# Kernel tuning notes

Hardware: AMD Instinct MI355X
Metric: run time of the kernel (lower is better)

## Reference

```python
import jax, jax.numpy as jnp
import numpy as np

T, B = 64, 2048
LATENT, OBS, CTRL, NMAT, H = 128, 128, 16, 16, 128


def setup_inputs() -> dict:
    key = jax.random.key(0)
    ks = iter(jax.random.split(key, 32))

    def dense(shape, fan_in):
        return jax.random.normal(next(ks), shape, jnp.float32) / np.sqrt(fan_in)

    inp = {
        "xs": jax.random.normal(next(ks), (T, B, OBS), jnp.float32),
        "us": jax.random.normal(next(ks), (T, B, CTRL), jnp.float32),
        "eps1": jax.random.normal(next(ks), (B, LATENT), jnp.float32),
        "eps": jax.random.normal(next(ks), (T - 1, B, LATENT), jnp.float32),
        # InitialNetwork: LSTM(128) + Dense(128) + Dense(2*latent)
        "lstm_Wx": dense((OBS, 4 * H), OBS),
        "lstm_Wh": dense((H, 4 * H), H),
        "lstm_b": jnp.zeros((4 * H,), jnp.float32),
        "init_W1": dense((H, H), H),
        "init_b1": jnp.zeros((H,), jnp.float32),
        "init_W2": dense((H, 2 * LATENT), H),
        "init_b2": jnp.zeros((2 * LATENT,), jnp.float32),
        # InitialTransition
        "trans_W1": dense((LATENT, H), LATENT),
        "trans_b1": jnp.zeros((H,), jnp.float32),
        "trans_W2": dense((H, LATENT), H),
        "trans_b2": jnp.zeros((LATENT,), jnp.float32),
        # Observation
        "obs_W1": dense((LATENT, H), LATENT),
        "obs_b1": jnp.zeros((H,), jnp.float32),
        "obs_W2": dense((H, OBS), H),
        "obs_b2": jnp.zeros((OBS,), jnp.float32),
        # Recognition (input: z ++ x ++ u)
        "rec_W1": dense((LATENT + OBS + CTRL, H), LATENT + OBS + CTRL),
        "rec_b1": jnp.zeros((H,), jnp.float32),
        "rec_W2": dense((H, 2 * LATENT), H),
        "rec_b2": jnp.zeros((2 * LATENT,), jnp.float32),
        # TransitionWeights (no bias, normal(0.01) init)
        "alpha_W": 0.01 * jax.random.normal(next(ks), (LATENT + CTRL, NMAT), jnp.float32),
        # mixture banks
        "A": 0.01 * jax.random.normal(next(ks), (NMAT, LATENT, LATENT), jnp.float32),
        "Bm": 0.01 * jax.random.normal(next(ks), (NMAT, LATENT, CTRL), jnp.float32),
        "C": 0.01 * jax.random.normal(next(ks), (NMAT, OBS, LATENT), jnp.float32),
    }
    return inp


def reference(xs, us, eps1, eps, lstm_Wx, lstm_Wh, lstm_b,
              init_W1, init_b1, init_W2, init_b2,
              trans_W1, trans_b1, trans_W2, trans_b2,
              obs_W1, obs_b1, obs_W2, obs_b2,
              rec_W1, rec_b1, rec_W2, rec_b2,
              alpha_W, A, Bm, C):
    Bsz = xs.shape[1]
    Hd = lstm_Wh.shape[0]

    # --- InitialNetwork: LSTM over time (xs is (T,B,obs); flax transposes to batch-major, net effect is a scan over T) ---
    def lstm_step(carry, x_t):
        c, h = carry
        gates = x_t @ lstm_Wx + h @ lstm_Wh + lstm_b  # (B, 4H)
        i, f, g, o = jnp.split(gates, 4, axis=-1)     # flax gate order i,f,g,o
        c = jax.nn.sigmoid(f) * c + jax.nn.sigmoid(i) * jnp.tanh(g)
        h = jax.nn.sigmoid(o) * jnp.tanh(c)
        return (c, h), None

    zeros = jnp.zeros((Bsz, Hd), xs.dtype)
    (_, h_last), _ = jax.lax.scan(lstm_step, (zeros, zeros), xs)
    hid = jax.nn.relu(h_last @ init_W1 + init_b1)
    w1_mean, w1_logvar = jnp.split(hid @ init_W2 + init_b2, 2, axis=-1)
    w_1 = w1_mean + jnp.exp(w1_logvar / 2) * eps1

    # --- InitialTransition ---
    z_1 = jax.nn.relu(w_1 @ trans_W1 + trans_b1) @ trans_W2 + trans_b2

    def obs_fn(z):
        return jax.nn.relu(z @ obs_W1 + obs_b1) @ obs_W2 + obs_b2

    # --- unrolled DVBF transition as a scan over t = 0..T-2 ---
    def step(z, inp):
        x_next, u_t, eps_t = inp
        x_mean = obs_fn(z)
        r = jax.nn.relu(jnp.concatenate([z, x_next, u_t], axis=-1) @ rec_W1 + rec_b1)
        w_mean, w_logvar = jnp.split(r @ rec_W2 + rec_b2, 2, axis=-1)
        w = w_mean + jnp.exp(w_logvar / 2) * eps_t
        alphas = jax.nn.softmax(jnp.concatenate([z, u_t], axis=-1) @ alpha_W)  # (B, NMAT)
        # fused gating + matrix mixing + matvec (same math as building A_t/B_t/C_t)
        z_next = (jnp.einsum('bi,ijk,bk->bj', alphas, A, z)
                  + jnp.einsum('bi,ijk,bk->bj', alphas, Bm, u_t)
                  + jnp.einsum('bi,ijk,bk->bj', alphas, C, w))
        return z_next, (z_next, x_mean)

    Tn = xs.shape[0]
    _, (zs_rest, x_rec) = jax.lax.scan(step, z_1, (xs[1:], us[:Tn - 1], eps[:Tn - 1]))

    zs = jnp.concatenate([z_1[None], zs_rest], axis=0).reshape(-1, z_1.shape[-1])  # vstack -> (T*B, latent)
    x_rec = x_rec.reshape(-1, x_rec.shape[-1])                                    # ((T-1)*B, obs)
    return zs, x_rec
```

## Files before the change

kernel.cpp:

```cpp
#include <hip/hip_runtime.h>
#include <math.h>

#define TT   64
#define BB   2048
#define OBSN 128
#define CTRLN 16
#define LATN 128
#define NMN  16
#define HDN  128

typedef __attribute__((ext_vector_type(8))) short short8;
typedef __attribute__((ext_vector_type(4))) float f32x4;

__device__ __forceinline__ float sigf(float x) { return 1.0f / (1.0f + expf(-x)); }

__device__ __forceinline__ unsigned short f2bf(float x) {
    unsigned int u = __float_as_uint(x);
    unsigned int r = (u + 0x7fffu + ((u >> 16) & 1u)) >> 16;
    return (unsigned short)r;
}

__device__ __forceinline__ f32x4 mfma16(short8 a, short8 b, f32x4 c) {
    return __builtin_amdgcn_mfma_f32_16x16x32_bf16(a, b, c, 0, 0, 0);
}

__global__ __launch_bounds__(256) void cvt_bf4_k(
    const float* __restrict__ in, unsigned short* __restrict__ out, int n4)
{
    int i = blockIdx.x * 256 + threadIdx.x;
    if (i >= n4) return;
    float4 v = ((const float4*)in)[i];
    ushort4 o;
    o.x = f2bf(v.x); o.y = f2bf(v.y); o.z = f2bf(v.z); o.w = f2bf(v.w);
    ((ushort4*)out)[i] = o;
}

__global__ __launch_bounds__(256) void pack_b_k(
    const float* __restrict__ W, unsigned short* __restrict__ out,
    int K, int N, int KT)
{
    int id = blockIdx.x * 256 + threadIdx.x;
    int total = (N / 16) * KT * 64;
    if (id >= total) return;
    int lane = id & 63;
    int kt = (id >> 6) % KT;
    int nt = id / (64 * KT);
    int n = nt * 16 + (lane & 15);
    int kb = kt * 32 + (lane >> 4) * 8;
#pragma unroll
    for (int j = 0; j < 8; j++) {
        int k = kb + j;
        out[(size_t)id * 8 + j] = (k < K) ? f2bf(W[(size_t)k * N + n]) : (unsigned short)0;
    }
}

__global__ __launch_bounds__(256) void pack_lstm_k(
    const float* __restrict__ Wx, const float* __restrict__ Wh,
    unsigned short* __restrict__ out)
{
    int id = blockIdx.x * 256 + threadIdx.x;
    if (id >= 32 * 8 * 64) return;
    int lane = id & 63;
    int kt = (id >> 6) & 7;
    int nt = id >> 9;
    int n = nt * 16 + (lane & 15);
    int kb = kt * 32 + (lane >> 4) * 8;
#pragma unroll
    for (int j = 0; j < 8; j++) {
        int k = kb + j;
        float v = (k < 128) ? Wx[(size_t)k * 512 + n] : Wh[(size_t)(k - 128) * 512 + n];
        out[(size_t)id * 8 + j] = f2bf(v);
    }
}

__global__ __launch_bounds__(256) void pack_wmix_k(
    const float* __restrict__ A, const float* __restrict__ Bm,
    const float* __restrict__ C, unsigned short* __restrict__ out)
{
    int id = blockIdx.x * 256 + threadIdx.x;
    if (id >= 128 * 9 * 64) return;
    int lane = id & 63;
    int kt = (id >> 6) % 9;
    int nt = id / (64 * 9);
    int c = nt * 16 + (lane & 15);
    int i = c >> 7, jj = c & 127;
    int kb = kt * 32 + (lane >> 4) * 8;
#pragma unroll
    for (int j = 0; j < 8; j++) {
        int k = kb + j;
        float v;
        if (k < 128)      v = A[((size_t)(i * 128 + jj)) * 128 + k];
        else if (k < 144) v = Bm[(size_t)(i * 128 + jj) * 16 + (k - 128)];
        else if (k < 272) v = C[(size_t)(i * 128 + jj) * 128 + (k - 144)];
        else              v = 0.f;
        out[(size_t)id * 8 + j] = f2bf(v);
    }
}

__global__ __launch_bounds__(512, 2) void lstm_k(
    const unsigned short* __restrict__ xs_bf,
    const unsigned short* __restrict__ lstm_pk,
    const float* __restrict__ bias,
    float* __restrict__ hlast)
{
    __shared__ unsigned short wl[13 * 8 * 64 * 8];
    __shared__ unsigned short h_bf[16][136];
    __shared__ float cs[16][128];
    __shared__ float gb[16][516];
    __shared__ float bs[512];

    const int tid = threadIdx.x;
    const int lane = tid & 63;
    const int w = tid >> 6;
    const int quad = lane >> 4;
    const int l15 = lane & 15;
    const int row0 = blockIdx.x * 16;

    short8 bl[19];
#pragma unroll
    for (int f = 0; f < 19; f++) {
        int s = f >> 3, kt = f & 7;
        bl[f] = *(const short8*)&lstm_pk[((((size_t)(w * 4 + s)) * 8 + kt) * 64 + lane) * 8];
    }
#pragma unroll
    for (int f = 19; f < 32; f++) {
        int s = f >> 3, kt = f & 7;
        *(short8*)&wl[(((size_t)w * 13 + (f - 19)) * 64 + lane) * 8] =
            *(const short8*)&lstm_pk[((((size_t)(w * 4 + s)) * 8 + kt) * 64 + lane) * 8];
    }

    bs[tid] = bias[tid];
    for (int idx = tid; idx < 16 * 136; idx += 512) h_bf[idx / 136][idx % 136] = 0;
    for (int idx = tid; idx < 2048; idx += 512) cs[idx >> 7][idx & 127] = 0.f;

    short8 axs[4];
#pragma unroll
    for (int kt = 0; kt < 4; kt++)
        axs[kt] = *(const short8*)&xs_bf[((size_t)(row0 + l15)) * 128 + kt * 32 + quad * 8];
    __syncthreads();

    for (int t = 0; t < TT; t++) {
        short8 a[8];
#pragma unroll
        for (int kt = 0; kt < 4; kt++) a[kt] = axs[kt];
#pragma unroll
        for (int kt = 4; kt < 8; kt++)
            a[kt] = *(const short8*)&h_bf[l15][(kt - 4) * 32 + quad * 8];

        f32x4 D[4];
#pragma unroll
        for (int s = 0; s < 4; s++) D[s] = (f32x4){0.f, 0.f, 0.f, 0.f};
#pragma unroll
        for (int s = 0; s < 4; s++) {
#pragma unroll
            for (int kt = 0; kt < 8; kt++) {
                int f = s * 8 + kt;
                short8 b;
                if (f < 19) b = bl[f];
                else        b = *(const short8*)&wl[(((size_t)w * 13 + (f - 19)) * 64 + lane) * 8];
                D[s] = mfma16(a[kt], b, D[s]);
            }
        }
#pragma unroll
        for (int s = 0; s < 4; s++)
#pragma unroll
            for (int rg = 0; rg < 4; rg++)
                gb[quad * 4 + rg][(w * 4 + s) * 16 + l15] = D[s][rg];
        __syncthreads();

        if (t + 1 < TT) {
#pragma unroll
            for (int kt = 0; kt < 4; kt++)
                axs[kt] = *(const short8*)&xs_bf[((size_t)(t + 1) * 2048 + row0 + l15) * 128 + kt * 32 + quad * 8];
        }
#pragma unroll
        for (int e = 0; e < 4; e++) {
            int idx = tid + e * 512;
            int r = idx >> 7, j = idx & 127;
            float gi = gb[r][j] + bs[j];
            float gf = gb[r][128 + j] + bs[128 + j];
            float gg = gb[r][256 + j] + bs[256 + j];
            float go = gb[r][384 + j] + bs[384 + j];
            float c = sigf(gf) * cs[r][j] + sigf(gi) * tanhf(gg);
            float h = sigf(go) * tanhf(c);
            cs[r][j] = c;
            h_bf[r][j] = f2bf(h);
            if (t == TT - 1) hlast[(size_t)(row0 + r) * 128 + j] = h;
        }
        __syncthreads();
    }
}

__global__ __launch_bounds__(512, 2) void scan_k(
    const unsigned short* __restrict__ xs_bf,
    const unsigned short* __restrict__ us_bf,
    const float* __restrict__ eps,
    const unsigned short* __restrict__ rec1_pk,
    const float* __restrict__ rec_b1,
    const unsigned short* __restrict__ rec2_pk,
    const float* __restrict__ rec_b2,
    const unsigned short* __restrict__ alpha_pk,
    const unsigned short* __restrict__ wmix_pk,
    float* __restrict__ zs)
{
    __shared__ unsigned short amix[16][296];
    __shared__ unsigned short rb_bf[16][136];
    __shared__ float wv[16][260];
    __shared__ float part[8][16][132];
    __shared__ float logits[16][20];
    __shared__ float alph[16][20];
    __shared__ float b1s[128];
    __shared__ float b2s[256];

    const int tid = threadIdx.x;
    const int lane = tid & 63;
    const int w = tid >> 6;
    const int quad = lane >> 4;
    const int l15 = lane & 15;
    const int row0 = blockIdx.x * 16;

    short8 r1f[9];
#pragma unroll
    for (int kt = 0; kt < 9; kt++)
        r1f[kt] = *(const short8*)&rec1_pk[(((size_t)w * 9 + kt) * 64 + lane) * 8];
    short8 r2f[8];
#pragma unroll
    for (int s = 0; s < 2; s++)
#pragma unroll
        for (int kt = 0; kt < 4; kt++)
            r2f[s * 4 + kt] = *(const short8*)&rec2_pk[((((size_t)(2 * w + s)) * 4 + kt) * 64 + lane) * 8];
    short8 alf[5];
#pragma unroll
    for (int kt = 0; kt < 5; kt++)
        alf[kt] = *(const short8*)&alpha_pk[((size_t)kt * 64 + lane) * 8];

    if (tid < 128) b1s[tid] = rec_b1[tid];
    if (tid < 256) b2s[tid] = rec_b2[tid];
    for (int idx = tid; idx < 256; idx += 512)
        amix[idx >> 4][272 + (idx & 15)] = 0;
    for (int idx = tid; idx < 2048; idx += 512) {
        int r = idx >> 7, j = idx & 127;
        amix[r][j] = f2bf(zs[(size_t)(row0 + r) * 128 + j]);
    }
    __syncthreads();

    float ge[4];
    short8 axs[4];

    for (int t = 0; t < TT - 1; t++) {
        if (tid < 256) {
            int r = tid >> 4, c = tid & 15;
            amix[r][128 + c] = us_bf[((size_t)t * 2048 + row0 + r) * 16 + c];
        }
#pragma unroll
        for (int e = 0; e < 4; e++) {
            int idx = tid + e * 512;
            int r = idx >> 7, j = idx & 127;
            ge[e] = eps[((size_t)t * 2048 + row0 + r) * 128 + j];
        }
#pragma unroll
        for (int kt = 0; kt < 4; kt++)
            axs[kt] = *(const short8*)&xs_bf[((size_t)(t + 1) * 2048 + row0 + l15) * 128 + kt * 32 + quad * 8];
        __syncthreads();

        {
            short8 a[9];
#pragma unroll
            for (int kt = 0; kt < 4; kt++)
                a[kt] = *(const short8*)&amix[l15][kt * 32 + quad * 8];
#pragma unroll
            for (int kt = 4; kt < 8; kt++) a[kt] = axs[kt - 4];
            {
                short8 zz = {0, 0, 0, 0, 0, 0, 0, 0};
                a[8] = (quad < 2) ? *(const short8*)&amix[l15][128 + quad * 8] : zz;
            }
            f32x4 D = {0.f, 0.f, 0.f, 0.f};
#pragma unroll
            for (int kt = 0; kt < 9; kt++)
                D = mfma16(a[kt], r1f[kt], D);
            int col = w * 16 + l15;
#pragma unroll
            for (int rg = 0; rg < 4; rg++) {
                float v = fmaxf(D[rg] + b1s[col], 0.f);
                rb_bf[quad * 4 + rg][col] = f2bf(v);
            }
        }
        __syncthreads();

        {
            short8 a[4];
#pragma unroll
            for (int kt = 0; kt < 4; kt++)
                a[kt] = *(const short8*)&rb_bf[l15][kt * 32 + quad * 8];
            f32x4 D0 = {0.f, 0.f, 0.f, 0.f}, D1 = {0.f, 0.f, 0.f, 0.f};
#pragma unroll
            for (int kt = 0; kt < 4; kt++) {
                D0 = mfma16(a[kt], r2f[kt], D0);
                D1 = mfma16(a[kt], r2f[4 + kt], D1);
            }
#pragma unroll
            for (int rg = 0; rg < 4; rg++) {
                wv[quad * 4 + rg][(2 * w) * 16 + l15] = D0[rg];
                wv[quad * 4 + rg][(2 * w + 1) * 16 + l15] = D1[rg];
            }
            if (w == 7) {
                short8 az[5];
#pragma unroll
                for (int kt = 0; kt < 4; kt++)
                    az[kt] = *(const short8*)&amix[l15][kt * 32 + quad * 8];
                short8 zz = {0, 0, 0, 0, 0, 0, 0, 0};
                az[4] = (quad < 2) ? *(const short8*)&amix[l15][128 + quad * 8] : zz;
                f32x4 DL = {0.f, 0.f, 0.f, 0.f};
#pragma unroll
                for (int kt = 0; kt < 5; kt++)
                    DL = mfma16(az[kt], alf[kt], DL);
#pragma unroll
                for (int rg = 0; rg < 4; rg++)
                    logits[quad * 4 + rg][l15] = DL[rg];
            }
        }
        __syncthreads();

        if (tid < 256) {
            int r = tid >> 4, i = tid & 15;
            float x = logits[r][i];
            float m = x;
#pragma unroll
            for (int off = 8; off > 0; off >>= 1)
                m = fmaxf(m, __shfl_xor(m, off, 16));
            float e = expf(x - m);
            float s = e;
#pragma unroll
            for (int off = 8; off > 0; off >>= 1)
                s += __shfl_xor(s, off, 16);
            alph[r][i] = e / s;
        }
#pragma unroll
        for (int e = 0; e < 4; e++) {
            int idx = tid + e * 512;
            int r = idx >> 7, j = idx & 127;
            float mv = wv[r][j] + b2s[j];
            float lv = wv[r][128 + j] + b2s[128 + j];
            float wval = mv + expf(0.5f * lv) * ge[e];
            amix[r][144 + j] = f2bf(wval);
        }
        __syncthreads();

        {
            short8 a[9];
#pragma unroll
            for (int kt = 0; kt < 9; kt++)
                a[kt] = *(const short8*)&amix[l15][kt * 32 + quad * 8];
            const int i0 = 2 * w, i1 = 2 * w + 1;
            float a0[4], a1[4];
#pragma unroll
            for (int rg = 0; rg < 4; rg++) {
                a0[rg] = alph[quad * 4 + rg][i0];
                a1[rg] = alph[quad * 4 + rg][i1];
            }
#pragma unroll 1
            for (int jt = 0; jt < 8; jt++) {
                f32x4 D0 = {0.f, 0.f, 0.f, 0.f}, D1 = {0.f, 0.f, 0.f, 0.f};
#pragma unroll
                for (int kt = 0; kt < 9; kt++) {
                    short8 b0 = *(const short8*)&wmix_pk[((((size_t)i0 * 8 + jt) * 9 + kt) * 64 + lane) * 8];
                    short8 b1 = *(const short8*)&wmix_pk[((((size_t)i1 * 8 + jt) * 9 + kt) * 64 + lane) * 8];
                    D0 = mfma16(a[kt], b0, D0);
                    D1 = mfma16(a[kt], b1, D1);
                }
#pragma unroll
                for (int rg = 0; rg < 4; rg++)
                    part[w][quad * 4 + rg][jt * 16 + l15] = a0[rg] * D0[rg] + a1[rg] * D1[rg];
            }
        }
        __syncthreads();

#pragma unroll
        for (int e = 0; e < 4; e++) {
            int idx = tid + e * 512;
            int r = idx >> 7, j = idx & 127;
            float s = 0.f;
#pragma unroll
            for (int ww = 0; ww < 8; ww++) s += part[ww][r][j];
            zs[((size_t)(t + 1) * 2048 + row0 + r) * 128 + j] = s;
            amix[r][j] = f2bf(s);
        }
        __syncthreads();
    }
}

template <int RELU>
__global__ __launch_bounds__(256) void gemm_bias_k(
    const float* __restrict__ A, const float* __restrict__ W,
    const float* __restrict__ bias, float* __restrict__ Cout,
    int M, int K, int N)
{
    __shared__ float As[16][68];
    __shared__ float Ws[16][64];
    const int tid = threadIdx.x;
    const int row0 = blockIdx.x * 64;
    const int col0 = blockIdx.y * 64;
    const int tx = tid & 15, ty = tid >> 4;
    float acc[4][4];
#pragma unroll
    for (int a = 0; a < 4; a++)
#pragma unroll
        for (int b = 0; b < 4; b++) acc[a][b] = 0.f;

    for (int kc = 0; kc < K; kc += 16) {
        __syncthreads();
#pragma unroll
        for (int e = 0; e < 4; e++) {
            int idx = tid + e * 256;
            int r = idx >> 4, kk = idx & 15;
            As[kk][r] = A[(size_t)(row0 + r) * K + kc + kk];
        }
#pragma unroll
        for (int e = 0; e < 4; e++) {
            int idx = tid + e * 256;
            int kk = idx >> 6, jj = idx & 63;
            Ws[kk][jj] = W[(kc + kk) * N + col0 + jj];
        }
        __syncthreads();
#pragma unroll
        for (int kk = 0; kk < 16; kk++) {
            const float4 a4 = *(const float4*)&As[kk][ty * 4];
            const float4 w4 = *(const float4*)&Ws[kk][tx * 4];
            const float av[4] = {a4.x, a4.y, a4.z, a4.w};
            const float wv2[4] = {w4.x, w4.y, w4.z, w4.w};
#pragma unroll
            for (int r = 0; r < 4; r++)
#pragma unroll
                for (int j = 0; j < 4; j++) acc[r][j] += av[r] * wv2[j];
        }
    }
#pragma unroll
    for (int r = 0; r < 4; r++)
#pragma unroll
        for (int j = 0; j < 4; j++) {
            int gr = row0 + ty * 4 + r, gc = col0 + tx * 4 + j;
            float v = acc[r][j] + bias[gc];
            if (RELU) v = fmaxf(v, 0.f);
            Cout[(size_t)gr * N + gc] = v;
        }
}

__global__ __launch_bounds__(256) void gemm_meanvar_k(
    const float* __restrict__ A, const float* __restrict__ W,
    const float* __restrict__ bias, const float* __restrict__ eps,
    float* __restrict__ out)
{
    __shared__ float As[16][36];
    __shared__ float Ws[16][128];
    const int tid = threadIdx.x;
    const int row0 = blockIdx.x * 32;
    const int j0 = blockIdx.y * 64;
    const int tjx = tid & 31;
    const int trg = tid >> 5;
    float am[4][2], al[4][2];
#pragma unroll
    for (int a = 0; a < 4; a++) { am[a][0] = am[a][1] = 0.f; al[a][0] = al[a][1] = 0.f; }

    for (int kc = 0; kc < 128; kc += 16) {
        __syncthreads();
#pragma unroll
        for (int e = 0; e < 2; e++) {
            int idx = tid + e * 256;
            int r = idx >> 4, kk = idx & 15;
            As[kk][r] = A[(row0 + r) * 128 + kc + kk];
        }
#pragma unroll
        for (int e = 0; e < 2; e++) {
            int idx = tid + e * 256;
            int lin = idx * 4;
            int kk = lin >> 7, cc = lin & 127;
            int half = cc >> 6, jj = cc & 63;
            *(float4*)&Ws[kk][half * 64 + jj] =
                *(const float4*)(W + (kc + kk) * 256 + half * 128 + j0 + jj);
        }
        __syncthreads();
#pragma unroll
        for (int kk = 0; kk < 16; kk++) {
            const float4 a4 = *(const float4*)&As[kk][trg * 4];
            const float2 wm = *(const float2*)&Ws[kk][2 * tjx];
            const float2 wl = *(const float2*)&Ws[kk][64 + 2 * tjx];
            const float av[4] = {a4.x, a4.y, a4.z, a4.w};
#pragma unroll
            for (int rr = 0; rr < 4; rr++) {
                am[rr][0] += av[rr] * wm.x; am[rr][1] += av[rr] * wm.y;
                al[rr][0] += av[rr] * wl.x; al[rr][1] += av[rr] * wl.y;
            }
        }
    }
#pragma unroll
    for (int rr = 0; rr < 4; rr++)
#pragma unroll
        for (int jj = 0; jj < 2; jj++) {
            int r = row0 + trg * 4 + rr;
            int j = j0 + 2 * tjx + jj;
            float m = am[rr][jj] + bias[j];
            float l = al[rr][jj] + bias[128 + j];
            out[r * 128 + j] = m + expf(0.5f * l) * eps[r * 128 + j];
        }
}

__global__ __launch_bounds__(256) void mlp2_k(
    const float* __restrict__ Z, const float* __restrict__ W1,
    const float* __restrict__ b1, const float* __restrict__ W2,
    const float* __restrict__ b2, float* __restrict__ out)
{
    __shared__ float Zs[32][132];
    __shared__ float Hs[32][132];
    __shared__ float Ws[16][128];
    const int tid = threadIdx.x;
    const int row0 = blockIdx.x * 32;
    const int tx = tid & 31;
    const int ty = tid >> 5;

#pragma unroll
    for (int e = 0; e < 4; e++) {
        int idx = tid + e * 256;
        int lin = idx * 4;
        int r = lin >> 7, k = lin & 127;
        *(float4*)&Zs[r][k] = *(const float4*)(Z + (size_t)(row0 + r) * 128 + k);
    }

    float acc[4][4];
#pragma unroll
    for (int a = 0; a < 4; a++)
#pragma unroll
        for (int b = 0; b < 4; b++) acc[a][b] = 0.f;

    for (int kc = 0; kc < 128; kc += 16) {
        __syncthreads();
#pragma unroll
        for (int e = 0; e < 2; e++) {
            int idx = tid + e * 256;
            int lin = idx * 4;
            int kk = lin >> 7, j = lin & 127;
            *(float4*)&Ws[kk][j] = *(const float4*)(W1 + (kc + kk) * 128 + j);
        }
        __syncthreads();
#pragma unroll
        for (int kk = 0; kk < 16; kk++) {
            float av[4];
#pragma unroll
            for (int rr = 0; rr < 4; rr++) av[rr] = Zs[ty * 4 + rr][kc + kk];
            const float4 w4 = *(const float4*)&Ws[kk][tx * 4];
            const float wv2[4] = {w4.x, w4.y, w4.z, w4.w};
#pragma unroll
            for (int r = 0; r < 4; r++)
#pragma unroll
                for (int j = 0; j < 4; j++) acc[r][j] += av[r] * wv2[j];
        }
    }
#pragma unroll
    for (int rr = 0; rr < 4; rr++) {
        float4 hv;
        hv.x = fmaxf(acc[rr][0] + b1[tx * 4 + 0], 0.f);
        hv.y = fmaxf(acc[rr][1] + b1[tx * 4 + 1], 0.f);
        hv.z = fmaxf(acc[rr][2] + b1[tx * 4 + 2], 0.f);
        hv.w = fmaxf(acc[rr][3] + b1[tx * 4 + 3], 0.f);
        *(float4*)&Hs[ty * 4 + rr][tx * 4] = hv;
    }
#pragma unroll
    for (int a = 0; a < 4; a++)
#pragma unroll
        for (int b = 0; b < 4; b++) acc[a][b] = 0.f;

    for (int kc = 0; kc < 128; kc += 16) {
        __syncthreads();
#pragma unroll
        for (int e = 0; e < 2; e++) {
            int idx = tid + e * 256;
            int lin = idx * 4;
            int kk = lin >> 7, j = lin & 127;
            *(float4*)&Ws[kk][j] = *(const float4*)(W2 + (kc + kk) * 128 + j);
        }
        __syncthreads();
#pragma unroll
        for (int kk = 0; kk < 16; kk++) {
            float av[4];
#pragma unroll
            for (int rr = 0; rr < 4; rr++) av[rr] = Hs[ty * 4 + rr][kc + kk];
            const float4 w4 = *(const float4*)&Ws[kk][tx * 4];
            const float wv2[4] = {w4.x, w4.y, w4.z, w4.w};
#pragma unroll
            for (int r = 0; r < 4; r++)
#pragma unroll
                for (int j = 0; j < 4; j++) acc[r][j] += av[r] * wv2[j];
        }
    }
#pragma unroll
    for (int rr = 0; rr < 4; rr++) {
        float4 ov;
        ov.x = acc[rr][0] + b2[tx * 4 + 0];
        ov.y = acc[rr][1] + b2[tx * 4 + 1];
        ov.z = acc[rr][2] + b2[tx * 4 + 2];
        ov.w = acc[rr][3] + b2[tx * 4 + 3];
        *(float4*)(out + (size_t)(row0 + ty * 4 + rr) * 128 + tx * 4) = ov;
    }
}

extern "C" void kernel_launch(void* const* d_in, const int* in_sizes, int n_in,
                              void* d_out, int out_size, void* d_ws, size_t ws_size,
                              hipStream_t stream)
{
    (void)in_sizes; (void)n_in; (void)out_size; (void)ws_size;
    const float* xs       = (const float*)d_in[0];
    const float* us       = (const float*)d_in[1];
    const float* eps1     = (const float*)d_in[2];
    const float* eps      = (const float*)d_in[3];
    const float* lstm_Wx  = (const float*)d_in[4];
    const float* lstm_Wh  = (const float*)d_in[5];
    const float* lstm_b   = (const float*)d_in[6];
    const float* init_W1  = (const float*)d_in[7];
    const float* init_b1  = (const float*)d_in[8];
    const float* init_W2  = (const float*)d_in[9];
    const float* init_b2  = (const float*)d_in[10];
    const float* trans_W1 = (const float*)d_in[11];
    const float* trans_b1 = (const float*)d_in[12];
    const float* trans_W2 = (const float*)d_in[13];
    const float* trans_b2 = (const float*)d_in[14];
    const float* obs_W1   = (const float*)d_in[15];
    const float* obs_b1   = (const float*)d_in[16];
    const float* obs_W2   = (const float*)d_in[17];
    const float* obs_b2   = (const float*)d_in[18];
    const float* rec_W1   = (const float*)d_in[19];
    const float* rec_b1   = (const float*)d_in[20];
    const float* rec_W2   = (const float*)d_in[21];
    const float* rec_b2   = (const float*)d_in[22];
    const float* alpha_W  = (const float*)d_in[23];
    const float* Amat     = (const float*)d_in[24];
    const float* Bmat     = (const float*)d_in[25];
    const float* Cmat     = (const float*)d_in[26];

    float* out  = (float*)d_out;
    float* zs   = out;
    float* xrec = out + (size_t)TT * BB * LATN;

    char* ws = (char*)d_ws;
    unsigned short* xs_bf   = (unsigned short*)(ws);
    unsigned short* us_bf   = (unsigned short*)(ws + 33554432);
    unsigned short* lstm_pk = (unsigned short*)(ws + 37748736);
    unsigned short* rec1_pk = (unsigned short*)(ws + 38010880);
    unsigned short* rec2_pk = (unsigned short*)(ws + 38084608);
    unsigned short* alpha_pk= (unsigned short*)(ws + 38150144);
    unsigned short* wmix_pk = (unsigned short*)(ws + 38155264);
    float* hlast            = (float*)(ws + 39334912);
    float* hidb             = (float*)(ws + 40383488);
    float* w1b              = (float*)(ws + 41432064);
    float* rbg              = (float*)(ws + 42480640);

    cvt_bf4_k<<<16384, 256, 0, stream>>>(xs, xs_bf, 4194304);
    cvt_bf4_k<<<2048, 256, 0, stream>>>(us, us_bf, 524288);
    pack_lstm_k<<<64, 256, 0, stream>>>(lstm_Wx, lstm_Wh, lstm_pk);
    pack_b_k<<<18, 256, 0, stream>>>(rec_W1, rec1_pk, 272, 128, 9);
    pack_b_k<<<16, 256, 0, stream>>>(rec_W2, rec2_pk, 128, 256, 4);
    pack_b_k<<<2, 256, 0, stream>>>(alpha_W, alpha_pk, 144, 16, 5);
    pack_wmix_k<<<288, 256, 0, stream>>>(Amat, Bmat, Cmat, wmix_pk);

    lstm_k<<<128, 512, 0, stream>>>(xs_bf, lstm_pk, lstm_b, hlast);

    gemm_bias_k<1><<<dim3(32, 2), 256, 0, stream>>>(hlast, init_W1, init_b1, hidb, BB, 128, 128);
    gemm_meanvar_k<<<dim3(64, 2), 256, 0, stream>>>(hidb, init_W2, init_b2, eps1, w1b);
    gemm_bias_k<1><<<dim3(32, 2), 256, 0, stream>>>(w1b, trans_W1, trans_b1, rbg, BB, 128, 128);
    gemm_bias_k<0><<<dim3(32, 2), 256, 0, stream>>>(rbg, trans_W2, trans_b2, zs, BB, 128, 128);

    scan_k<<<128, 512, 0, stream>>>(xs_bf, us_bf, eps,
                                    rec1_pk, rec_b1, rec2_pk, rec_b2,
                                    alpha_pk, wmix_pk, zs);

    mlp2_k<<<dim3((TT - 1) * BB / 32), 256, 0, stream>>>(
        zs, obs_W1, obs_b1, obs_W2, obs_b2, xrec);
}
```

Measured before the change: 1.329 ms.

## Overlap A/B mixture matmul with recognition net via warp specialization in scan

The scan kernel splits its warps: four warps compute the alpha-weighted A·z + B·u mixture while the other four run the recognition MLP, so the two independent parts of each step overlap. The mixture weights are split into separate A/B and C packs, the C·w term is computed afterwards by all warps, and the softmax for the next step is computed at the end of the current step. rec_W2 fragments now sit in LDS and several barriers and the logits/wv staging are removed. The cost is load imbalance between the warp groups and more LDS per block, which may lower occupancy.

```diff
diff --git a/kernel.cpp b/kernel.cpp
--- a/kernel.cpp
+++ b/kernel.cpp
@@ -73,15 +73,15 @@
     }
 }
 
-__global__ __launch_bounds__(256) void pack_wmix_k(
+__global__ __launch_bounds__(256) void pack_ab_k(
     const float* __restrict__ A, const float* __restrict__ Bm,
-    const float* __restrict__ C, unsigned short* __restrict__ out)
+    unsigned short* __restrict__ out)
 {
     int id = blockIdx.x * 256 + threadIdx.x;
-    if (id >= 128 * 9 * 64) return;
+    if (id >= 128 * 5 * 64) return;
     int lane = id & 63;
-    int kt = (id >> 6) % 9;
-    int nt = id / (64 * 9);
+    int kt = (id >> 6) % 5;
+    int nt = id / (64 * 5);
     int c = nt * 16 + (lane & 15);
     int i = c >> 7, jj = c & 127;
     int kb = kt * 32 + (lane >> 4) * 8;
@@ -91,9 +91,26 @@
         float v;
         if (k < 128)      v = A[((size_t)(i * 128 + jj)) * 128 + k];
         else if (k < 144) v = Bm[(size_t)(i * 128 + jj) * 16 + (k - 128)];
-        else if (k < 272) v = C[(size_t)(i * 128 + jj) * 128 + (k - 144)];
         else              v = 0.f;
         out[(size_t)id * 8 + j] = f2bf(v);
+    }
+}
+
+__global__ __launch_bounds__(256) void pack_c_k(
+    const float* __restrict__ C, unsigned short* __restrict__ out)
+{
+    int id = blockIdx.x * 256 + threadIdx.x;
+    if (id >= 128 * 4 * 64) return;
+    int lane = id & 63;
+    int kt = (id >> 6) & 3;
+    int nt = id >> 8;
+    int c = nt * 16 + (lane & 15);
+    int i = c >> 7, jj = c & 127;
+    int kb = kt * 32 + (lane >> 4) * 8;
+#pragma unroll
+    for (int j = 0; j < 8; j++) {
+        int k = kb + j;
+        out[(size_t)id * 8 + j] = f2bf(C[((size_t)(i * 128 + jj)) * 128 + k]);
     }
 }
 
@@ -200,15 +217,15 @@
     const unsigned short* __restrict__ rec2_pk,
     const float* __restrict__ rec_b2,
     const unsigned short* __restrict__ alpha_pk,
-    const unsigned short* __restrict__ wmix_pk,
+    const unsigned short* __restrict__ ab_pk,
+    const unsigned short* __restrict__ c_pk,
     float* __restrict__ zs)
 {
     __shared__ unsigned short amix[16][296];
     __shared__ unsigned short rb_bf[16][136];
-    __shared__ float wv[16][260];
-    __shared__ float part[8][16][132];
-    __shared__ float logits[16][20];
-    __shared__ float alph[16][20];
+    __shared__ unsigned short r2lds[16 * 4 * 64 * 8];
+    __shared__ float part1[8][16][16];
+    __shared__ float alph[16][17];
     __shared__ float b1s[128];
     __shared__ float b2s[256];
 
@@ -218,172 +235,259 @@
     const int quad = lane >> 4;
     const int l15 = lane & 15;
     const int row0 = blockIdx.x * 16;
-
-    short8 r1f[9];
-#pragma unroll
-    for (int kt = 0; kt < 9; kt++)
-        r1f[kt] = *(const short8*)&rec1_pk[(((size_t)w * 9 + kt) * 64 + lane) * 8];
-    short8 r2f[8];
-#pragma unroll
-    for (int s = 0; s < 2; s++)
-#pragma unroll
-        for (int kt = 0; kt < 4; kt++)
-            r2f[s * 4 + kt] = *(const short8*)&rec2_pk[((((size_t)(2 * w + s)) * 4 + kt) * 64 + lane) * 8];
+    const int s = w - 4;
+
+    short8 r1f[2][9];
     short8 alf[5];
-#pragma unroll
-    for (int kt = 0; kt < 5; kt++)
-        alf[kt] = *(const short8*)&alpha_pk[((size_t)kt * 64 + lane) * 8];
+    float ge[8];
+    short8 axs[4];
+
+    if (w >= 4) {
+#pragma unroll
+        for (int q = 0; q < 2; q++) {
+            int nt = s + 4 * q;
+#pragma unroll
+            for (int kt = 0; kt < 9; kt++)
+                r1f[q][kt] = *(const short8*)&rec1_pk[(((size_t)nt * 9 + kt) * 64 + lane) * 8];
+        }
+        if (w == 4) {
+#pragma unroll
+            for (int kt = 0; kt < 5; kt++)
+                alf[kt] = *(const short8*)&alpha_pk[((size_t)kt * 64 + lane) * 8];
+        }
+    }
+
+    for (int idx = tid; idx < 4096; idx += 512)
+        ((short8*)r2lds)[idx] = ((const short8*)rec2_pk)[idx];
 
     if (tid < 128) b1s[tid] = rec_b1[tid];
     if (tid < 256) b2s[tid] = rec_b2[tid];
-    for (int idx = tid; idx < 256; idx += 512)
-        amix[idx >> 4][272 + (idx & 15)] = 0;
     for (int idx = tid; idx < 2048; idx += 512) {
         int r = idx >> 7, j = idx & 127;
         amix[r][j] = f2bf(zs[(size_t)(row0 + r) * 128 + j]);
     }
+    if (tid < 256) {
+        int r = tid >> 4, c = tid & 15;
+        amix[r][128 + c] = us_bf[((size_t)(row0 + r)) * 16 + c];
+    }
+    for (int idx = tid; idx < 16 * 152; idx += 512) {
+        int r = idx / 152, j = idx % 152;
+        amix[r][144 + j] = 0;
+    }
     __syncthreads();
 
-    float ge[4];
-    short8 axs[4];
+    if (w == 4) {
+        short8 az[5];
+#pragma unroll
+        for (int kt = 0; kt < 4; kt++)
+            az[kt] = *(const short8*)&amix[l15][kt * 32 + quad * 8];
+        short8 zz = {0, 0, 0, 0, 0, 0, 0, 0};
+        az[4] = (quad < 2) ? *(const short8*)&amix[l15][128 + quad * 8] : zz;
+        f32x4 DL = {0.f, 0.f, 0.f, 0.f};
+#pragma unroll
+        for (int kt = 0; kt < 5; kt++) DL = mfma16(az[kt], alf[kt], DL);
+#pragma unroll
+        for (int rg = 0; rg < 4; rg++) {
+            float x = DL[rg];
+            float m = x;
+#pragma unroll
+            for (int off = 8; off > 0; off >>= 1) m = fmaxf(m, __shfl_xor(m, off, 16));
+            float e = expf(x - m);
+            float ssum = e;
+#pragma unroll
+            for (int off = 8; off > 0; off >>= 1) ssum += __shfl_xor(ssum, off, 16);
+            alph[quad * 4 + rg][l15] = e / ssum;
+        }
+    }
+    if (w >= 4) {
+#pragma unroll
+        for (int jj = 0; jj < 2; jj++)
+#pragma unroll
+            for (int rg = 0; rg < 4; rg++)
+                ge[jj * 4 + rg] = eps[((size_t)(row0 + quad * 4 + rg)) * 128 + (2 * s + jj) * 16 + l15];
+#pragma unroll
+        for (int kt = 0; kt < 4; kt++)
+            axs[kt] = *(const short8*)&xs_bf[((size_t)2048 + row0 + l15) * 128 + kt * 32 + quad * 8];
+    }
+    __syncthreads();
+
+    short8 a1[5];
+    f32x4 accj0, accj1;
 
     for (int t = 0; t < TT - 1; t++) {
-        if (tid < 256) {
-            int r = tid >> 4, c = tid & 15;
-            amix[r][128 + c] = us_bf[((size_t)t * 2048 + row0 + r) * 16 + c];
-        }
-#pragma unroll
-        for (int e = 0; e < 4; e++) {
-            int idx = tid + e * 512;
-            int r = idx >> 7, j = idx & 127;
-            ge[e] = eps[((size_t)t * 2048 + row0 + r) * 128 + j];
-        }
-#pragma unroll
-        for (int kt = 0; kt < 4; kt++)
-            axs[kt] = *(const short8*)&xs_bf[((size_t)(t + 1) * 2048 + row0 + l15) * 128 + kt * 32 + quad * 8];
-        __syncthreads();
-
-        {
-            short8 a[9];
+        if (w < 4) {
+#pragma unroll
+            for (int kt = 0; kt < 5; kt++)
+                a1[kt] = *(const short8*)&amix[l15][kt * 32 + quad * 8];
+            accj0 = (f32x4){0.f, 0.f, 0.f, 0.f};
+            accj1 = (f32x4){0.f, 0.f, 0.f, 0.f};
+#pragma unroll 2
+            for (int i = 0; i < 8; i++) {
+                f32x4 D0 = {0.f, 0.f, 0.f, 0.f}, D1 = {0.f, 0.f, 0.f, 0.f};
+#pragma unroll
+                for (int kt = 0; kt < 5; kt++) {
+                    short8 b0 = *(const short8*)&ab_pk[((((size_t)i * 8 + 2 * w) * 5 + kt) * 64 + lane) * 8];
+                    short8 b1 = *(const short8*)&ab_pk[((((size_t)i * 8 + 2 * w + 1) * 5 + kt) * 64 + lane) * 8];
+                    D0 = mfma16(a1[kt], b0, D0);
+                    D1 = mfma16(a1[kt], b1, D1);
+                }
+#pragma unroll
+                for (int rg = 0; rg < 4; rg++) {
+                    float al = alph[quad * 4 + rg][i];
+                    accj0[rg] += al * D0[rg];
+                    accj1[rg] += al * D1[rg];
+                }
+            }
+        } else {
+            short8 ar[9];
 #pragma unroll
             for (int kt = 0; kt < 4; kt++)
-                a[kt] = *(const short8*)&amix[l15][kt * 32 + quad * 8];
-#pragma unroll
-            for (int kt = 4; kt < 8; kt++) a[kt] = axs[kt - 4];
+                ar[kt] = *(const short8*)&amix[l15][kt * 32 + quad * 8];
+#pragma unroll
+            for (int kt = 4; kt < 8; kt++) ar[kt] = axs[kt - 4];
             {
                 short8 zz = {0, 0, 0, 0, 0, 0, 0, 0};
-                a[8] = (quad < 2) ? *(const short8*)&amix[l15][128 + quad * 8] : zz;
-            }
-            f32x4 D = {0.f, 0.f, 0.f, 0.f};
-#pragma unroll
-            for (int kt = 0; kt < 9; kt++)
-                D = mfma16(a[kt], r1f[kt], D);
-            int col = w * 16 + l15;
+                ar[8] = (quad < 2) ? *(const short8*)&amix[l15][128 + quad * 8] : zz;
+            }
+#pragma unroll
+            for (int q = 0; q < 2; q++) {
+                int nt = s + 4 * q;
+                f32x4 D = {0.f, 0.f, 0.f, 0.f};
+#pragma unroll
+                for (int kt = 0; kt < 9; kt++) D = mfma16(ar[kt], r1f[q][kt], D);
+                int col = nt * 16 + l15;
+#pragma unroll
+                for (int rg = 0; rg < 4; rg++)
+                    rb_bf[quad * 4 + rg][col] = f2bf(fmaxf(D[rg] + b1s[col], 0.f));
+            }
+        }
+        __syncthreads();
+
+        if (w < 4) {
+#pragma unroll 2
+            for (int i = 8; i < 16; i++) {
+                f32x4 D0 = {0.f, 0.f, 0.f, 0.f}, D1 = {0.f, 0.f, 0.f, 0.f};
+#pragma unroll
+                for (int kt = 0; kt < 5; kt++) {
+                    short8 b0 = *(const short8*)&ab_pk[((((size_t)i * 8 + 2 * w) * 5 + kt) * 64 + lane) * 8];
+                    short8 b1 = *(const short8*)&ab_pk[((((size_t)i * 8 + 2 * w + 1) * 5 + kt) * 64 + lane) * 8];
+                    D0 = mfma16(a1[kt], b0, D0);
+                    D1 = mfma16(a1[kt], b1, D1);
+                }
+#pragma unroll
+                for (int rg = 0; rg < 4; rg++) {
+                    float al = alph[quad * 4 + rg][i];
+                    accj0[rg] += al * D0[rg];
+                    accj1[rg] += al * D1[rg];
+                }
+            }
 #pragma unroll
             for (int rg = 0; rg < 4; rg++) {
-                float v = fmaxf(D[rg] + b1s[col], 0.f);
-                rb_bf[quad * 4 + rg][col] = f2bf(v);
+                part1[2 * w][quad * 4 + rg][l15] = accj0[rg];
+                part1[2 * w + 1][quad * 4 + rg][l15] = accj1[rg];
+            }
+        } else {
+            short8 a2[4];
+#pragma unroll
+            for (int kt = 0; kt < 4; kt++)
+                a2[kt] = *(const short8*)&rb_bf[l15][kt * 32 + quad * 8];
+            f32x4 Dm[2], Dl[2];
+#pragma unroll
+            for (int jj = 0; jj < 2; jj++) {
+                int ntm = 2 * s + jj;
+                int ntl = 2 * s + 8 + jj;
+                f32x4 D0 = {0.f, 0.f, 0.f, 0.f}, D1 = {0.f, 0.f, 0.f, 0.f};
+#pragma unroll
+                for (int kt = 0; kt < 4; kt++) {
+                    short8 bm = *(const short8*)&r2lds[(((size_t)ntm * 4 + kt) * 64 + lane) * 8];
+                    short8 bv = *(const short8*)&r2lds[(((size_t)ntl * 4 + kt) * 64 + lane) * 8];
+                    D0 = mfma16(a2[kt], bm, D0);
+                    D1 = mfma16(a2[kt], bv, D1);
+                }
+                Dm[jj] = D0; Dl[jj] = D1;
+            }
+#pragma unroll
+            for (int jj = 0; jj < 2; jj++) {
+                int col = (2 * s + jj) * 16 + l15;
+#pragma unroll
+                for (int rg = 0; rg < 4; rg++) {
+                    float mv = Dm[jj][rg] + b2s[col];
+                    float lv = Dl[jj][rg] + b2s[128 + col];
+                    float wval = mv + expf(0.5f * lv) * ge[jj * 4 + rg];
+                    amix[quad * 4 + rg][144 + col] = f2bf(wval);
+                }
             }
         }
         __syncthreads();
 
         {
-            short8 a[4];
+            short8 a2f[4];
 #pragma unroll
             for (int kt = 0; kt < 4; kt++)
-                a[kt] = *(const short8*)&rb_bf[l15][kt * 32 + quad * 8];
-            f32x4 D0 = {0.f, 0.f, 0.f, 0.f}, D1 = {0.f, 0.f, 0.f, 0.f};
-#pragma unroll
-            for (int kt = 0; kt < 4; kt++) {
-                D0 = mfma16(a[kt], r2f[kt], D0);
-                D1 = mfma16(a[kt], r2f[4 + kt], D1);
+                a2f[kt] = *(const short8*)&amix[l15][144 + kt * 32 + quad * 8];
+            f32x4 accC = {0.f, 0.f, 0.f, 0.f};
+#pragma unroll 2
+            for (int i = 0; i < 16; i++) {
+                f32x4 D = {0.f, 0.f, 0.f, 0.f};
+#pragma unroll
+                for (int kt = 0; kt < 4; kt++) {
+                    short8 b = *(const short8*)&c_pk[((((size_t)i * 8 + w) * 4 + kt) * 64 + lane) * 8];
+                    D = mfma16(a2f[kt], b, D);
+                }
+#pragma unroll
+                for (int rg = 0; rg < 4; rg++)
+                    accC[rg] += alph[quad * 4 + rg][i] * D[rg];
             }
 #pragma unroll
             for (int rg = 0; rg < 4; rg++) {
-                wv[quad * 4 + rg][(2 * w) * 16 + l15] = D0[rg];
-                wv[quad * 4 + rg][(2 * w + 1) * 16 + l15] = D1[rg];
-            }
-            if (w == 7) {
+                int r = quad * 4 + rg;
+                float z = part1[w][r][l15] + accC[rg];
+                zs[((size_t)(t + 1) * 2048 + row0 + r) * 128 + w * 16 + l15] = z;
+                amix[r][w * 16 + l15] = f2bf(z);
+            }
+        }
+        __syncthreads();
+
+        if (t < TT - 2) {
+            if (w == 4) {
                 short8 az[5];
 #pragma unroll
                 for (int kt = 0; kt < 4; kt++)
                     az[kt] = *(const short8*)&amix[l15][kt * 32 + quad * 8];
                 short8 zz = {0, 0, 0, 0, 0, 0, 0, 0};
-                az[4] = (quad < 2) ? *(const short8*)&amix[l15][128 + quad * 8] : zz;
+                az[4] = (quad < 2)
+                    ? *(const short8*)&us_bf[((size_t)(t + 1) * 2048 + row0 + l15) * 16 + quad * 8]
+                    : zz;
                 f32x4 DL = {0.f, 0.f, 0.f, 0.f};
 #pragma unroll
-                for (int kt = 0; kt < 5; kt++)
-                    DL = mfma16(az[kt], alf[kt], DL);
-#pragma unroll
-                for (int rg = 0; rg < 4; rg++)
-                    logits[quad * 4 + rg][l15] = DL[rg];
-            }
-        }
-        __syncthreads();
-
-        if (tid < 256) {
-            int r = tid >> 4, i = tid & 15;
-            float x = logits[r][i];
-            float m = x;
-#pragma unroll
-            for (int off = 8; off > 0; off >>= 1)
-                m = fmaxf(m, __shfl_xor(m, off, 16));
-            float e = expf(x - m);
-            float s = e;
-#pragma unroll
-            for (int off = 8; off > 0; off >>= 1)
-                s += __shfl_xor(s, off, 16);
-            alph[r][i] = e / s;
-        }
-#pragma unroll
-        for (int e = 0; e < 4; e++) {
-            int idx = tid + e * 512;
-            int r = idx >> 7, j = idx & 127;
-            float mv = wv[r][j] + b2s[j];
-            float lv = wv[r][128 + j] + b2s[128 + j];
-            float wval = mv + expf(0.5f * lv) * ge[e];
-            amix[r][144 + j] = f2bf(wval);
-        }
-        __syncthreads();
-
-        {
-            short8 a[9];
-#pragma unroll
-            for (int kt = 0; kt < 9; kt++)
-                a[kt] = *(const short8*)&amix[l15][kt * 32 + quad * 8];
-            const int i0 = 2 * w, i1 = 2 * w + 1;
-            float a0[4], a1[4];
-#pragma unroll
-            for (int rg = 0; rg < 4; rg++) {
-                a0[rg] = alph[quad * 4 + rg][i0];
-                a1[rg] = alph[quad * 4 + rg][i1];
-            }
-#pragma unroll 1
-            for (int jt = 0; jt < 8; jt++) {
-                f32x4 D0 = {0.f, 0.f, 0.f, 0.f}, D1 = {0.f, 0.f, 0.f, 0.f};
-#pragma unroll
-                for (int kt = 0; kt < 9; kt++) {
-                    short8 b0 = *(const short8*)&wmix_pk[((((size_t)i0 * 8 + jt) * 9 + kt) * 64 + lane) * 8];
-                    short8 b1 = *(const short8*)&wmix_pk[((((size_t)i1 * 8 + jt) * 9 + kt) * 64 + lane) * 8];
-                    D0 = mfma16(a[kt], b0, D0);
-                    D1 = mfma16(a[kt], b1, D1);
+                for (int kt = 0; kt < 5; kt++) DL = mfma16(az[kt], alf[kt], DL);
+#pragma unroll
+                for (int rg = 0; rg < 4; rg++) {
+                    float x = DL[rg];
+                    float m = x;
+#pragma unroll
+                    for (int off = 8; off > 0; off >>= 1) m = fmaxf(m, __shfl_xor(m, off, 16));
+                    float e = expf(x - m);
+                    float ssum = e;
+#pragma unroll
+                    for (int off = 8; off > 0; off >>= 1) ssum += __shfl_xor(ssum, off, 16);
+                    alph[quad * 4 + rg][l15] = e / ssum;
                 }
-#pragma unroll
-                for (int rg = 0; rg < 4; rg++)
-                    part[w][quad * 4 + rg][jt * 16 + l15] = a0[rg] * D0[rg] + a1[rg] * D1[rg];
-            }
-        }
-        __syncthreads();
-
-#pragma unroll
-        for (int e = 0; e < 4; e++) {
-            int idx = tid + e * 512;
-            int r = idx >> 7, j = idx & 127;
-            float s = 0.f;
-#pragma unroll
-            for (int ww = 0; ww < 8; ww++) s += part[ww][r][j];
-            zs[((size_t)(t + 1) * 2048 + row0 + r) * 128 + j] = s;
-            amix[r][j] = f2bf(s);
+            }
+            if (tid < 256) {
+                int r = tid >> 4, c = tid & 15;
+                amix[r][128 + c] = us_bf[((size_t)(t + 1) * 2048 + row0 + r) * 16 + c];
+            }
+            if (w >= 4) {
+#pragma unroll
+                for (int jj = 0; jj < 2; jj++)
+#pragma unroll
+                    for (int rg = 0; rg < 4; rg++)
+                        ge[jj * 4 + rg] = eps[((size_t)(t + 1) * 2048 + row0 + quad * 4 + rg) * 128 + (2 * s + jj) * 16 + l15];
+#pragma unroll
+                for (int kt = 0; kt < 4; kt++)
+                    axs[kt] = *(const short8*)&xs_bf[((size_t)(t + 2) * 2048 + row0 + l15) * 128 + kt * 32 + quad * 8];
+            }
         }
         __syncthreads();
     }
@@ -646,7 +750,8 @@
     unsigned short* rec1_pk = (unsigned short*)(ws + 38010880);
     unsigned short* rec2_pk = (unsigned short*)(ws + 38084608);
     unsigned short* alpha_pk= (unsigned short*)(ws + 38150144);
-    unsigned short* wmix_pk = (unsigned short*)(ws + 38155264);
+    unsigned short* ab_pk   = (unsigned short*)(ws + 38155264);
+    unsigned short* c_pk    = (unsigned short*)(ws + 38810624);
     float* hlast            = (float*)(ws + 39334912);
     float* hidb             = (float*)(ws + 40383488);
     float* w1b              = (float*)(ws + 41432064);
@@ -658,7 +763,8 @@
     pack_b_k<<<18, 256, 0, stream>>>(rec_W1, rec1_pk, 272, 128, 9);
     pack_b_k<<<16, 256, 0, stream>>>(rec_W2, rec2_pk, 128, 256, 4);
     pack_b_k<<<2, 256, 0, stream>>>(alpha_W, alpha_pk, 144, 16, 5);
-    pack_wmix_k<<<288, 256, 0, stream>>>(Amat, Bmat, Cmat, wmix_pk);
+    pack_ab_k<<<160, 256, 0, stream>>>(Amat, Bmat, ab_pk);
+    pack_c_k<<<128, 256, 0, stream>>>(Cmat, c_pk);
 
     lstm_k<<<128, 512, 0, stream>>>(xs_bf, lstm_pk, lstm_b, hlast);
 
@@ -669,7 +775,7 @@
 
     scan_k<<<128, 512, 0, stream>>>(xs_bf, us_bf, eps,
                                     rec1_pk, rec_b1, rec2_pk, rec_b2,
-                                    alpha_pk, wmix_pk, zs);
+                                    alpha_pk, ab_pk, c_pk, zs);
 
     mlp2_k<<<dim3((TT - 1) * BB / 32), 256, 0, stream>>>(
         zs, obs_W1, obs_b1, obs_W2, obs_b2, xrec);
```

Result: slower. 1.696 ms (+27.6%).

## Cache mixing weights in registers/LDS and fuse reparameterization into rec2 epilogue

Applied to the files above, without the earlier changes.

Part of the per-step mixture weight bank (first three k-tiles for matrix i0 and the first k-tile for i1) is preloaded once into registers and shared memory. This cuts repeated global/L2 reads inside the 63-step scan. The rec_W2 column mapping is reordered so each wave computes matching mean and logvar columns. That lets the sample w be formed directly in the MFMA epilogue, removing the wv shared buffer and a separate elementwise pass. The cost is much higher register pressure (24 extra short8), which risks spills or lower occupancy under launch_bounds(512,2), and the jt loop is now fully unrolled.

```diff
diff --git a/kernel.cpp b/kernel.cpp
--- a/kernel.cpp
+++ b/kernel.cpp
@@ -205,7 +205,7 @@
 {
     __shared__ unsigned short amix[16][296];
     __shared__ unsigned short rb_bf[16][136];
-    __shared__ float wv[16][260];
+    __shared__ unsigned short wl1[8][8][64 * 8];
     __shared__ float part[8][16][132];
     __shared__ float logits[16][20];
     __shared__ float alph[16][20];
@@ -218,6 +218,7 @@
     const int quad = lane >> 4;
     const int l15 = lane & 15;
     const int row0 = blockIdx.x * 16;
+    const int i0 = 2 * w, i1 = 2 * w + 1;
 
     short8 r1f[9];
 #pragma unroll
@@ -225,14 +226,25 @@
         r1f[kt] = *(const short8*)&rec1_pk[(((size_t)w * 9 + kt) * 64 + lane) * 8];
     short8 r2f[8];
 #pragma unroll
-    for (int s = 0; s < 2; s++)
-#pragma unroll
-        for (int kt = 0; kt < 4; kt++)
-            r2f[s * 4 + kt] = *(const short8*)&rec2_pk[((((size_t)(2 * w + s)) * 4 + kt) * 64 + lane) * 8];
+    for (int kt = 0; kt < 4; kt++) {
+        r2f[kt]     = *(const short8*)&rec2_pk[((((size_t)w) * 4 + kt) * 64 + lane) * 8];
+        r2f[4 + kt] = *(const short8*)&rec2_pk[((((size_t)(8 + w)) * 4 + kt) * 64 + lane) * 8];
+    }
     short8 alf[5];
 #pragma unroll
     for (int kt = 0; kt < 5; kt++)
         alf[kt] = *(const short8*)&alpha_pk[((size_t)kt * 64 + lane) * 8];
+
+    short8 wreg[24];
+#pragma unroll
+    for (int jt = 0; jt < 8; jt++) {
+#pragma unroll
+        for (int kt = 0; kt < 3; kt++)
+            wreg[jt * 3 + kt] =
+                *(const short8*)&wmix_pk[((((size_t)i0 * 8 + jt) * 9 + kt) * 64 + lane) * 8];
+        *(short8*)&wl1[w][jt][lane * 8] =
+            *(const short8*)&wmix_pk[((((size_t)i1 * 8 + jt) * 9 + 0) * 64 + lane) * 8];
+    }
 
     if (tid < 128) b1s[tid] = rec_b1[tid];
     if (tid < 256) b2s[tid] = rec_b2[tid];
@@ -253,11 +265,8 @@
             amix[r][128 + c] = us_bf[((size_t)t * 2048 + row0 + r) * 16 + c];
         }
 #pragma unroll
-        for (int e = 0; e < 4; e++) {
-            int idx = tid + e * 512;
-            int r = idx >> 7, j = idx & 127;
-            ge[e] = eps[((size_t)t * 2048 + row0 + r) * 128 + j];
-        }
+        for (int rg = 0; rg < 4; rg++)
+            ge[rg] = eps[((size_t)t * 2048 + row0 + quad * 4 + rg) * 128 + w * 16 + l15];
 #pragma unroll
         for (int kt = 0; kt < 4; kt++)
             axs[kt] = *(const short8*)&xs_bf[((size_t)(t + 1) * 2048 + row0 + l15) * 128 + kt * 32 + quad * 8];
@@ -288,20 +297,23 @@
         __syncthreads();
 
         {
-            short8 a[4];
+            short8 a2[4];
 #pragma unroll
             for (int kt = 0; kt < 4; kt++)
-                a[kt] = *(const short8*)&rb_bf[l15][kt * 32 + quad * 8];
-            f32x4 D0 = {0.f, 0.f, 0.f, 0.f}, D1 = {0.f, 0.f, 0.f, 0.f};
+                a2[kt] = *(const short8*)&rb_bf[l15][kt * 32 + quad * 8];
+            f32x4 Dm = {0.f, 0.f, 0.f, 0.f}, Dl = {0.f, 0.f, 0.f, 0.f};
 #pragma unroll
             for (int kt = 0; kt < 4; kt++) {
-                D0 = mfma16(a[kt], r2f[kt], D0);
-                D1 = mfma16(a[kt], r2f[4 + kt], D1);
-            }
+                Dm = mfma16(a2[kt], r2f[kt], Dm);
+                Dl = mfma16(a2[kt], r2f[4 + kt], Dl);
+            }
+            int col = w * 16 + l15;
 #pragma unroll
             for (int rg = 0; rg < 4; rg++) {
-                wv[quad * 4 + rg][(2 * w) * 16 + l15] = D0[rg];
-                wv[quad * 4 + rg][(2 * w + 1) * 16 + l15] = D1[rg];
+                float mv = Dm[rg] + b2s[col];
+                float lv = Dl[rg] + b2s[128 + col];
+                float wval = mv + expf(0.5f * lv) * ge[rg];
+                amix[quad * 4 + rg][144 + col] = f2bf(wval);
             }
             if (w == 7) {
                 short8 az[5];
@@ -335,15 +347,6 @@
                 s += __shfl_xor(s, off, 16);
             alph[r][i] = e / s;
         }
-#pragma unroll
-        for (int e = 0; e < 4; e++) {
-            int idx = tid + e * 512;
-            int r = idx >> 7, j = idx & 127;
-            float mv = wv[r][j] + b2s[j];
-            float lv = wv[r][128 + j] + b2s[128 + j];
-            float wval = mv + expf(0.5f * lv) * ge[e];
-            amix[r][144 + j] = f2bf(wval);
-        }
         __syncthreads();
 
         {
@@ -351,26 +354,29 @@
 #pragma unroll
             for (int kt = 0; kt < 9; kt++)
                 a[kt] = *(const short8*)&amix[l15][kt * 32 + quad * 8];
-            const int i0 = 2 * w, i1 = 2 * w + 1;
-            float a0[4], a1[4];
+            float a0[4], a1v[4];
 #pragma unroll
             for (int rg = 0; rg < 4; rg++) {
                 a0[rg] = alph[quad * 4 + rg][i0];
-                a1[rg] = alph[quad * 4 + rg][i1];
-            }
-#pragma unroll 1
+                a1v[rg] = alph[quad * 4 + rg][i1];
+            }
+#pragma unroll
             for (int jt = 0; jt < 8; jt++) {
                 f32x4 D0 = {0.f, 0.f, 0.f, 0.f}, D1 = {0.f, 0.f, 0.f, 0.f};
 #pragma unroll
                 for (int kt = 0; kt < 9; kt++) {
-                    short8 b0 = *(const short8*)&wmix_pk[((((size_t)i0 * 8 + jt) * 9 + kt) * 64 + lane) * 8];
-                    short8 b1 = *(const short8*)&wmix_pk[((((size_t)i1 * 8 + jt) * 9 + kt) * 64 + lane) * 8];
+                    short8 b0 = (kt < 3)
+                        ? wreg[jt * 3 + kt]
+                        : *(const short8*)&wmix_pk[((((size_t)i0 * 8 + jt) * 9 + kt) * 64 + lane) * 8];
+                    short8 b1 = (kt == 0)
+                        ? *(const short8*)&wl1[w][jt][lane * 8]
+                        : *(const short8*)&wmix_pk[((((size_t)i1 * 8 + jt) * 9 + kt) * 64 + lane) * 8];
                     D0 = mfma16(a[kt], b0, D0);
                     D1 = mfma16(a[kt], b1, D1);
                 }
 #pragma unroll
                 for (int rg = 0; rg < 4; rg++)
-                    part[w][quad * 4 + rg][jt * 16 + l15] = a0[rg] * D0[rg] + a1[rg] * D1[rg];
+                    part[w][quad * 4 + rg][jt * 16 + l15] = a0[rg] * D0[rg] + a1v[rg] * D1[rg];
             }
         }
         __syncthreads();
```

New measurement: 3.281 ms. 2.47x slower.
